# Optimization experiments

Hardware: AMD Instinct MI355X
Metric: run time of the kernel (lower is better)

Reference implementation:

```python
import jax, jax.numpy as jnp
import numpy as np

N_EXPERTS = 8
TOP_K = 2
D_MODEL = 1024
N_TOKENS = 8192


def setup_inputs() -> dict:
    key = jax.random.key(0)
    k1, k2, k3, k4, k5 = jax.random.split(key, 5)
    x = jax.random.normal(k1, (N_TOKENS, D_MODEL), dtype=jnp.float32)
    # router Linear(num_experts): weight [d, E], bias [E]
    Wr = jax.random.normal(k2, (D_MODEL, N_EXPERTS), dtype=jnp.float32) / np.sqrt(D_MODEL)
    br = jnp.zeros((N_EXPERTS,), dtype=jnp.float32)
    # per-expert Linear(d_model): stacked weights [E, d, d], biases [E, d]
    W = jax.random.normal(k3, (N_EXPERTS, D_MODEL, D_MODEL), dtype=jnp.float32) / np.sqrt(D_MODEL)
    b = jnp.zeros((N_EXPERTS, D_MODEL), dtype=jnp.float32)
    return {"x": x, "Wr": Wr, "br": br, "W": W, "b": b}


def reference(x, Wr, br, W, b):
    # --- route ---
    logits = x @ Wr + br                                  # [N, E]
    top_k_vals, top_k_idxs = jax.lax.top_k(logits, TOP_K)  # [N, k]
    top_k_gates = jax.nn.softmax(top_k_vals, axis=-1)      # [N, k]
    # --- experts (dense form of gather-dispatch; same math as routed compute) ---
    y_all = jnp.einsum('nd,edh->neh', x, W) + b            # [N, E, d]
    # --- gather routed expert outputs per slot ---
    y_k = jnp.take_along_axis(y_all, top_k_idxs[:, :, None], axis=1)  # [N, k, d]
    # --- weighted scatter-combine (reduce) ---
    out = jnp.sum(top_k_gates[:, :, None] * y_k, axis=1)   # [N, d]
    return out
```

## Files before the change

kernel.cpp:

```cpp
#include <hip/hip_runtime.h>
#include <hip/hip_bf16.h>


#define NTOK 8192
#define DM   1024
#define NEXP 8
#define CAP  8192
#define MAXT 136

typedef __attribute__((ext_vector_type(8))) short bf16x8;
typedef __attribute__((ext_vector_type(4))) float f32x4;

__device__ __forceinline__ unsigned short f2bf(float f) {
  unsigned u = __float_as_uint(f);
  unsigned r = (u + 0x7fffu + ((u >> 16) & 1u)) >> 16;
  return (unsigned short)r;
}
__device__ __forceinline__ float bf2f(unsigned short s) {
  return __uint_as_float(((unsigned)s) << 16);
}

__device__ __forceinline__ void gl_lds16(const void* g, void* l) {
  __builtin_amdgcn_global_load_lds(
      (const __attribute__((address_space(1))) unsigned int*)g,
      (__attribute__((address_space(3))) unsigned int*)l, 16, 0, 0);
}

__global__ __launch_bounds__(256) void transpose_w_kernel(
    const float* __restrict__ W, unsigned short* __restrict__ Wt) {
  __shared__ unsigned short L[64 * 260];
  const int e = blockIdx.z;
  const int d0 = blockIdx.y * 256, h0 = blockIdx.x * 64;
  const float* Ws = W + (size_t)e * DM * DM;
  unsigned short* Wd = Wt + (size_t)e * DM * DM;
  const int tid = threadIdx.x;
  const int hh = (tid & 15) * 4;
  const int dr = tid >> 4;
#pragma unroll
  for (int it = 0; it < 16; it++) {
    int dd = it * 16 + dr;
    float4 v = *(const float4*)(Ws + (size_t)(d0 + dd) * DM + h0 + hh);
    L[(hh + 0) * 260 + dd] = f2bf(v.x);
    L[(hh + 1) * 260 + dd] = f2bf(v.y);
    L[(hh + 2) * 260 + dd] = f2bf(v.z);
    L[(hh + 3) * 260 + dd] = f2bf(v.w);
  }
  __syncthreads();
  const int dc = (tid & 63) * 4;
  const int hw = tid >> 6;
#pragma unroll
  for (int it = 0; it < 16; it++) {
    int hr = it * 4 + hw;
    ushort4 o = *(const ushort4*)(&L[hr * 260 + dc]);
    *(ushort4*)(Wd + (size_t)(h0 + hr) * DM + d0 + dc) = o;
  }
}

__global__ __launch_bounds__(256) void router_compute_kernel(
    const float* __restrict__ x, const float* __restrict__ Wr,
    const float* __restrict__ br, unsigned short* __restrict__ xbf,
    int4* __restrict__ topk) {
  const int tid = threadIdx.x;
  const int wave = tid >> 6, lane = tid & 63;
  const int t = blockIdx.x * 4 + wave;
  const int c0 = lane * 16;
  const float* xr = x + (size_t)t * DM + c0;

  float v[16];
#pragma unroll
  for (int i = 0; i < 4; i++) {
    float4 f = *(const float4*)(xr + i * 4);
    v[i * 4 + 0] = f.x; v[i * 4 + 1] = f.y; v[i * 4 + 2] = f.z; v[i * 4 + 3] = f.w;
  }
  union { unsigned short s[8]; uint4 q; } pk;
#pragma unroll
  for (int half = 0; half < 2; half++) {
#pragma unroll
    for (int i = 0; i < 8; i++) pk.s[i] = f2bf(v[half * 8 + i]);
    *(uint4*)(xbf + (size_t)t * DM + c0 + half * 8) = pk.q;
  }
  float p[8] = {0, 0, 0, 0, 0, 0, 0, 0};
  const float* wr = Wr + (size_t)c0 * NEXP;
#pragma unroll
  for (int i = 0; i < 16; i++) {
    float xv = v[i];
    float4 wl = *(const float4*)(wr + i * 8);
    float4 wh = *(const float4*)(wr + i * 8 + 4);
    p[0] += xv * wl.x; p[1] += xv * wl.y; p[2] += xv * wl.z; p[3] += xv * wl.w;
    p[4] += xv * wh.x; p[5] += xv * wh.y; p[6] += xv * wh.z; p[7] += xv * wh.w;
  }
#pragma unroll
  for (int off = 32; off >= 1; off >>= 1) {
#pragma unroll
    for (int e = 0; e < 8; e++) p[e] += __shfl_xor(p[e], off, 64);
  }
  if (lane == 0) {
    float lg[8];
#pragma unroll
    for (int e = 0; e < 8; e++) lg[e] = p[e] + br[e];
    float v0 = lg[0]; int i0 = 0;
#pragma unroll
    for (int e = 1; e < 8; e++) if (lg[e] > v0) { v0 = lg[e]; i0 = e; }
    float v1 = -3.4e38f; int i1 = 0;
#pragma unroll
    for (int e = 0; e < 8; e++)
      if (e != i0 && lg[e] > v1) { v1 = lg[e]; i1 = e; }
    float ee = __expf(v1 - v0);
    float g0 = 1.0f / (1.0f + ee);
    float g1 = ee / (1.0f + ee);
    int4 rec;
    rec.x = i0; rec.y = i1;
    rec.z = __float_as_int(g0); rec.w = __float_as_int(g1);
    topk[t] = rec;
  }
}

__global__ __launch_bounds__(512) void scatter_kernel(
    const int4* __restrict__ topk, int* __restrict__ counts,
    int* __restrict__ tok, int2* __restrict__ pos) {
  __shared__ int lcnt[NEXP], lbase[NEXP];
  const int tid = threadIdx.x;
  if (tid < NEXP) lcnt[tid] = 0;
  __syncthreads();
  const int t = blockIdx.x * 512 + tid;
  int4 r = topk[t];
  int s0 = atomicAdd(&lcnt[r.x], 1);
  int s1 = atomicAdd(&lcnt[r.y], 1);
  __syncthreads();
  if (tid < NEXP) lbase[tid] = atomicAdd(&counts[tid], lcnt[tid]);
  __syncthreads();
  int p0 = lbase[r.x] + s0;
  int p1 = lbase[r.y] + s1;
  tok[r.x * CAP + p0] = t;
  tok[r.y * CAP + p1] = t;
  int2 pr; pr.x = p0; pr.y = p1;
  pos[t] = pr;
}

__global__ __launch_bounds__(64) void build_tiles_kernel(
    const int* __restrict__ counts, int* __restrict__ desc,
    int* __restrict__ ntiles, int* __restrict__ offset) {
  if (threadIdx.x == 0) {
    int idx = 0, off = 0;
#pragma unroll
    for (int e = 0; e < NEXP; e++) {
      offset[e] = off;
      off += counts[e];
      int nm = (counts[e] + 127) >> 7;
      for (int i = 0; i < nm; i++) desc[idx++] = (e << 16) | i;
    }
    *ntiles = idx;
  }
}

__global__ __launch_bounds__(256) void moe_gemm_kernel(
    const unsigned short* __restrict__ xbf, const unsigned short* __restrict__ wt,
    const int* __restrict__ counts, const int* __restrict__ offset,
    const int* __restrict__ tok, const int* __restrict__ desc,
    const int* __restrict__ ntiles, unsigned short* __restrict__ ybuf) {
  const int slot = blockIdx.x;
  if (slot >= *ntiles) return;
  const int dsc = desc[slot];
  const int e = dsc >> 16;
  const int m0 = (dsc & 0xffff) * 128;
  const int cnt = counts[e];
  const int n0 = blockIdx.y * 128;

  __shared__ __align__(16) unsigned short sA0[128 * 32];
  __shared__ __align__(16) unsigned short sB0[128 * 32];
  __shared__ __align__(16) unsigned short sA1[128 * 32];
  __shared__ __align__(16) unsigned short sB1[128 * 32];

  const int tid = threadIdx.x, wave = tid >> 6, lane = tid & 63;

  const int rA1 = wave * 16 + (lane >> 2);
  const int rA2 = rA1 + 64;
  const int cch = lane & 3;
  const int cg1 = (cch ^ ((rA1 >> 1) & 3)) * 8;
  const int cg2 = (cch ^ ((rA2 >> 1) & 3)) * 8;
  int r1 = m0 + rA1; if (r1 >= cnt) r1 = cnt - 1;
  int r2 = m0 + rA2; if (r2 >= cnt) r2 = cnt - 1;
  const int t1 = tok[e * CAP + r1];
  const int t2 = tok[e * CAP + r2];
  const unsigned short* pA1 = xbf + (size_t)t1 * DM + cg1;
  const unsigned short* pA2 = xbf + (size_t)t2 * DM + cg2;
  const unsigned short* wte = wt + (size_t)e * DM * DM;
  const unsigned short* pB1 = wte + (size_t)(n0 + rA1) * DM + cg1;
  const unsigned short* pB2 = wte + (size_t)(n0 + rA2) * DM + cg2;
  const int lo1 = wave * 512, lo2 = (wave + 4) * 512;

  const int q = lane >> 4, ml = lane & 15;
  const int wm = (wave >> 1) * 64, wn = (wave & 1) * 64;
  int offA[4], offB[4];
#pragma unroll
  for (int i = 0; i < 4; i++) {
    int row = wm + i * 16 + ml;
    offA[i] = row * 32 + (q ^ ((row >> 1) & 3)) * 8;
    int rowb = wn + i * 16 + ml;
    offB[i] = rowb * 32 + (q ^ ((rowb >> 1) & 3)) * 8;
  }

  f32x4 acc[4][4] = {};

  for (int k0 = 0; k0 < DM; k0 += 64) {
    gl_lds16(pA1 + k0, sA0 + lo1);
    gl_lds16(pA2 + k0, sA0 + lo2);
    gl_lds16(pB1 + k0, sB0 + lo1);
    gl_lds16(pB2 + k0, sB0 + lo2);
    gl_lds16(pA1 + k0 + 32, sA1 + lo1);
    gl_lds16(pA2 + k0 + 32, sA1 + lo2);
    gl_lds16(pB1 + k0 + 32, sB1 + lo1);
    gl_lds16(pB2 + k0 + 32, sB1 + lo2);
    __syncthreads();
    bf16x8 af0[4], bf0[4], af1[4], bf1[4];
#pragma unroll
    for (int i = 0; i < 4; i++) {
      af0[i] = *(const bf16x8*)(sA0 + offA[i]);
      bf0[i] = *(const bf16x8*)(sB0 + offB[i]);
      af1[i] = *(const bf16x8*)(sA1 + offA[i]);
      bf1[i] = *(const bf16x8*)(sB1 + offB[i]);
    }
#pragma unroll
    for (int mt = 0; mt < 4; mt++)
#pragma unroll
      for (int nt = 0; nt < 4; nt++)
        acc[mt][nt] = __builtin_amdgcn_mfma_f32_16x16x32_bf16(
            af0[mt], bf0[nt], acc[mt][nt], 0, 0, 0);
#pragma unroll
    for (int mt = 0; mt < 4; mt++)
#pragma unroll
      for (int nt = 0; nt < 4; nt++)
        acc[mt][nt] = __builtin_amdgcn_mfma_f32_16x16x32_bf16(
            af1[mt], bf1[nt], acc[mt][nt], 0, 0, 0);
    __syncthreads();
  }

  const int yb = offset[e] + m0;
#pragma unroll
  for (int mt = 0; mt < 4; mt++) {
    int rbase = wm + mt * 16 + q * 4;
#pragma unroll
    for (int r = 0; r < 4; r++) {
      int row = rbase + r;
      if (m0 + row >= cnt) continue;
      unsigned short* yrow = ybuf + (size_t)(yb + row) * DM + n0;
#pragma unroll
      for (int nt = 0; nt < 4; nt++) {
        yrow[wn + nt * 16 + ml] = f2bf(acc[mt][nt][r]);
      }
    }
  }
}

__global__ __launch_bounds__(256) void combine_kernel(
    const unsigned short* __restrict__ ybuf, const int4* __restrict__ topk,
    const int2* __restrict__ pos, const int* __restrict__ offset,
    const float* __restrict__ bias, float* __restrict__ out) {
  const int t = blockIdx.x;
  const int c = threadIdx.x * 4;
  int4 r = topk[t];
  int2 p = pos[t];
  float g0 = __int_as_float(r.z), g1 = __int_as_float(r.w);
  int s0 = offset[r.x] + p.x;
  int s1 = offset[r.y] + p.y;
  ushort4 ya = *(const ushort4*)(ybuf + (size_t)s0 * DM + c);
  ushort4 yb = *(const ushort4*)(ybuf + (size_t)s1 * DM + c);
  float4 b0 = *(const float4*)(bias + (size_t)r.x * DM + c);
  float4 b1 = *(const float4*)(bias + (size_t)r.y * DM + c);
  float4 o;
  o.x = g0 * (bf2f(ya.x) + b0.x) + g1 * (bf2f(yb.x) + b1.x);
  o.y = g0 * (bf2f(ya.y) + b0.y) + g1 * (bf2f(yb.y) + b1.y);
  o.z = g0 * (bf2f(ya.z) + b0.z) + g1 * (bf2f(yb.z) + b1.z);
  o.w = g0 * (bf2f(ya.w) + b0.w) + g1 * (bf2f(yb.w) + b1.w);
  *(float4*)(out + (size_t)t * DM + c) = o;
}

extern "C" void kernel_launch(void* const* d_in, const int* in_sizes, int n_in,
                              void* d_out, int out_size, void* d_ws, size_t ws_size,
                              hipStream_t stream) {
  const float* x  = (const float*)d_in[0];
  const float* Wr = (const float*)d_in[1];
  const float* br = (const float*)d_in[2];
  const float* W  = (const float*)d_in[3];
  const float* b  = (const float*)d_in[4];
  float* out = (float*)d_out;

  char* ws = (char*)d_ws;
  unsigned short* xbf  = (unsigned short*)ws;
  unsigned short* wt   = (unsigned short*)(ws + (16u << 20));
  unsigned short* ybuf = (unsigned short*)(ws + (32u << 20));
  char* ctrl = ws + (64u << 20);
  int*   counts = (int*)ctrl;
  int*   ntiles = (int*)(ctrl + 64);
  int*   offset = (int*)(ctrl + 128);
  int*   desc   = (int*)(ctrl + 256);
  int*   tok    = (int*)(ctrl + 4096);
  int2*  pos    = (int2*)(ctrl + 4096 + (256u << 10));
  int4*  topk   = (int4*)(ctrl + 4096 + (320u << 10));

  hipMemsetAsync(counts, 0, 128, stream);

  transpose_w_kernel<<<dim3(16, 4, 8), 256, 0, stream>>>(W, wt);
  router_compute_kernel<<<NTOK / 4, 256, 0, stream>>>(x, Wr, br, xbf, topk);
  scatter_kernel<<<16, 512, 0, stream>>>(topk, counts, tok, pos);
  build_tiles_kernel<<<1, 64, 0, stream>>>(counts, desc, ntiles, offset);
  moe_gemm_kernel<<<dim3(MAXT, 8), 256, 0, stream>>>(
      xbf, wt, counts, offset, tok, desc, ntiles, ybuf);
  combine_kernel<<<NTOK, 256, 0, stream>>>(ybuf, topk, pos, offset, b, out);
}
```

Measured before the change: 215.1 us.

## Fuse prepass kernels, drop memset and tile-build launch, compute offsets inline

Merges the weight transpose/convert and router into a single prepass kernel, which also clears the expert counts, replacing a memset and two launches. The tile descriptor build kernel is removed: each GEMM block derives its expert, row offset and output base directly from counts. The combine kernel computes offsets from counts itself and assigns one wave per token. The GEMM grid is reordered so consecutive blocks share an M-tile. This cuts launch count and serial tiny kernels, at the cost of redundant per-block prefix computations.

After: 215.1 us. About the same (-0.0%).

```diff
diff --git a/kernel.cpp b/kernel.cpp
--- a/kernel.cpp
+++ b/kernel.cpp
@@ -26,43 +26,48 @@
       (__attribute__((address_space(3))) unsigned int*)l, 16, 0, 0);
 }
 
-__global__ __launch_bounds__(256) void transpose_w_kernel(
-    const float* __restrict__ W, unsigned short* __restrict__ Wt) {
-  __shared__ unsigned short L[64 * 260];
-  const int e = blockIdx.z;
-  const int d0 = blockIdx.y * 256, h0 = blockIdx.x * 64;
-  const float* Ws = W + (size_t)e * DM * DM;
-  unsigned short* Wd = Wt + (size_t)e * DM * DM;
-  const int tid = threadIdx.x;
-  const int hh = (tid & 15) * 4;
-  const int dr = tid >> 4;
-#pragma unroll
-  for (int it = 0; it < 16; it++) {
-    int dd = it * 16 + dr;
-    float4 v = *(const float4*)(Ws + (size_t)(d0 + dd) * DM + h0 + hh);
-    L[(hh + 0) * 260 + dd] = f2bf(v.x);
-    L[(hh + 1) * 260 + dd] = f2bf(v.y);
-    L[(hh + 2) * 260 + dd] = f2bf(v.z);
-    L[(hh + 3) * 260 + dd] = f2bf(v.w);
-  }
-  __syncthreads();
-  const int dc = (tid & 63) * 4;
-  const int hw = tid >> 6;
-#pragma unroll
-  for (int it = 0; it < 16; it++) {
-    int hr = it * 4 + hw;
-    ushort4 o = *(const ushort4*)(&L[hr * 260 + dc]);
-    *(ushort4*)(Wd + (size_t)(h0 + hr) * DM + d0 + dc) = o;
-  }
-}
-
-__global__ __launch_bounds__(256) void router_compute_kernel(
+__global__ __launch_bounds__(256) void prepass_kernel(
+    const float* __restrict__ W, unsigned short* __restrict__ Wt,
     const float* __restrict__ x, const float* __restrict__ Wr,
     const float* __restrict__ br, unsigned short* __restrict__ xbf,
-    int4* __restrict__ topk) {
+    int4* __restrict__ topk, int* __restrict__ counts) {
+  __shared__ unsigned short L[64 * 132];
+  const int bx = blockIdx.x;
   const int tid = threadIdx.x;
+
+  if (bx == 0 && tid < NEXP) counts[tid] = 0;
+
+  if (bx < 1024) {
+    const int e = bx & 7;
+    const int d0 = ((bx >> 3) & 7) * 128;
+    const int h0 = (bx >> 6) * 64;
+    const float* Ws = W + (size_t)e * DM * DM;
+    unsigned short* Wd = Wt + (size_t)e * DM * DM;
+    const int hh = (tid & 15) * 4;
+    const int dr = tid >> 4;
+#pragma unroll
+    for (int it = 0; it < 8; it++) {
+      int dd = it * 16 + dr;
+      float4 v = *(const float4*)(Ws + (size_t)(d0 + dd) * DM + h0 + hh);
+      L[(hh + 0) * 132 + dd] = f2bf(v.x);
+      L[(hh + 1) * 132 + dd] = f2bf(v.y);
+      L[(hh + 2) * 132 + dd] = f2bf(v.z);
+      L[(hh + 3) * 132 + dd] = f2bf(v.w);
+    }
+    __syncthreads();
+    const int dc = (tid & 31) * 4;
+    const int hw = tid >> 5;
+#pragma unroll
+    for (int it = 0; it < 8; it++) {
+      int hr = it * 8 + hw;
+      ushort4 o = *(const ushort4*)(&L[hr * 132 + dc]);
+      *(ushort4*)(Wd + (size_t)(h0 + hr) * DM + d0 + dc) = o;
+    }
+    return;
+  }
+
   const int wave = tid >> 6, lane = tid & 63;
-  const int t = blockIdx.x * 4 + wave;
+  const int t = (bx - 1024) * 4 + wave;
   const int c0 = lane * 16;
   const float* xr = x + (size_t)t * DM + c0;
 
@@ -137,34 +142,26 @@
   pos[t] = pr;
 }
 
-__global__ __launch_bounds__(64) void build_tiles_kernel(
-    const int* __restrict__ counts, int* __restrict__ desc,
-    int* __restrict__ ntiles, int* __restrict__ offset) {
-  if (threadIdx.x == 0) {
-    int idx = 0, off = 0;
-#pragma unroll
-    for (int e = 0; e < NEXP; e++) {
-      offset[e] = off;
-      off += counts[e];
-      int nm = (counts[e] + 127) >> 7;
-      for (int i = 0; i < nm; i++) desc[idx++] = (e << 16) | i;
-    }
-    *ntiles = idx;
-  }
-}
-
 __global__ __launch_bounds__(256) void moe_gemm_kernel(
     const unsigned short* __restrict__ xbf, const unsigned short* __restrict__ wt,
-    const int* __restrict__ counts, const int* __restrict__ offset,
-    const int* __restrict__ tok, const int* __restrict__ desc,
-    const int* __restrict__ ntiles, unsigned short* __restrict__ ybuf) {
-  const int slot = blockIdx.x;
-  if (slot >= *ntiles) return;
-  const int dsc = desc[slot];
-  const int e = dsc >> 16;
-  const int m0 = (dsc & 0xffff) * 128;
-  const int cnt = counts[e];
-  const int n0 = blockIdx.y * 128;
+    const int* __restrict__ counts, const int* __restrict__ tok,
+    unsigned short* __restrict__ ybuf) {
+  const int slot = blockIdx.y;
+  int e = 0, m0 = 0, yb0 = 0, cnt = 0;
+  {
+    int tacc = 0, oacc = 0, found = 0;
+#pragma unroll
+    for (int ee = 0; ee < NEXP; ee++) {
+      int c = counts[ee];
+      int nm = (c + 127) >> 7;
+      if (!found && slot < tacc + nm) {
+        e = ee; m0 = (slot - tacc) * 128; yb0 = oacc; cnt = c; found = 1;
+      }
+      tacc += nm; oacc += c;
+    }
+    if (!found) return;
+  }
+  const int n0 = blockIdx.x * 128;
 
   __shared__ __align__(16) unsigned short sA0[128 * 32];
   __shared__ __align__(16) unsigned short sB0[128 * 32];
@@ -235,7 +232,7 @@
     __syncthreads();
   }
 
-  const int yb = offset[e] + m0;
+  const int yb = yb0 + m0;
 #pragma unroll
   for (int mt = 0; mt < 4; mt++) {
     int rbase = wm + mt * 16 + q * 4;
@@ -254,25 +251,40 @@
 
 __global__ __launch_bounds__(256) void combine_kernel(
     const unsigned short* __restrict__ ybuf, const int4* __restrict__ topk,
-    const int2* __restrict__ pos, const int* __restrict__ offset,
+    const int2* __restrict__ pos, const int* __restrict__ counts,
     const float* __restrict__ bias, float* __restrict__ out) {
-  const int t = blockIdx.x;
-  const int c = threadIdx.x * 4;
+  const int tid = threadIdx.x;
+  const int wave = tid >> 6, lane = tid & 63;
+  const int t = blockIdx.x * 4 + wave;
   int4 r = topk[t];
   int2 p = pos[t];
+  int off0 = 0, off1 = 0;
+#pragma unroll
+  for (int e = 0; e < NEXP; e++) {
+    int c = counts[e];
+    if (e < r.x) off0 += c;
+    if (e < r.y) off1 += c;
+  }
   float g0 = __int_as_float(r.z), g1 = __int_as_float(r.w);
-  int s0 = offset[r.x] + p.x;
-  int s1 = offset[r.y] + p.y;
-  ushort4 ya = *(const ushort4*)(ybuf + (size_t)s0 * DM + c);
-  ushort4 yb = *(const ushort4*)(ybuf + (size_t)s1 * DM + c);
-  float4 b0 = *(const float4*)(bias + (size_t)r.x * DM + c);
-  float4 b1 = *(const float4*)(bias + (size_t)r.y * DM + c);
-  float4 o;
-  o.x = g0 * (bf2f(ya.x) + b0.x) + g1 * (bf2f(yb.x) + b1.x);
-  o.y = g0 * (bf2f(ya.y) + b0.y) + g1 * (bf2f(yb.y) + b1.y);
-  o.z = g0 * (bf2f(ya.z) + b0.z) + g1 * (bf2f(yb.z) + b1.z);
-  o.w = g0 * (bf2f(ya.w) + b0.w) + g1 * (bf2f(yb.w) + b1.w);
-  *(float4*)(out + (size_t)t * DM + c) = o;
+  const unsigned short* y0 = ybuf + (size_t)(off0 + p.x) * DM + lane * 16;
+  const unsigned short* y1 = ybuf + (size_t)(off1 + p.y) * DM + lane * 16;
+  const float* b0 = bias + (size_t)r.x * DM + lane * 16;
+  const float* b1 = bias + (size_t)r.y * DM + lane * 16;
+  float* orow = out + (size_t)t * DM + lane * 16;
+  union { ushort4 u4; unsigned short s[4]; } ya, yb;
+#pragma unroll
+  for (int j = 0; j < 4; j++) {
+    ya.u4 = *(const ushort4*)(y0 + j * 4);
+    yb.u4 = *(const ushort4*)(y1 + j * 4);
+    float4 c0 = *(const float4*)(b0 + j * 4);
+    float4 c1 = *(const float4*)(b1 + j * 4);
+    float4 o;
+    o.x = g0 * (bf2f(ya.s[0]) + c0.x) + g1 * (bf2f(yb.s[0]) + c1.x);
+    o.y = g0 * (bf2f(ya.s[1]) + c0.y) + g1 * (bf2f(yb.s[1]) + c1.y);
+    o.z = g0 * (bf2f(ya.s[2]) + c0.z) + g1 * (bf2f(yb.s[2]) + c1.z);
+    o.w = g0 * (bf2f(ya.s[3]) + c0.w) + g1 * (bf2f(yb.s[3]) + c1.w);
+    *(float4*)(orow + j * 4) = o;
+  }
 }
 
 extern "C" void kernel_launch(void* const* d_in, const int* in_sizes, int n_in,
@@ -291,20 +303,15 @@
   unsigned short* ybuf = (unsigned short*)(ws + (32u << 20));
   char* ctrl = ws + (64u << 20);
   int*   counts = (int*)ctrl;
-  int*   ntiles = (int*)(ctrl + 64);
-  int*   offset = (int*)(ctrl + 128);
-  int*   desc   = (int*)(ctrl + 256);
   int*   tok    = (int*)(ctrl + 4096);
   int2*  pos    = (int2*)(ctrl + 4096 + (256u << 10));
   int4*  topk   = (int4*)(ctrl + 4096 + (320u << 10));
 
-  hipMemsetAsync(counts, 0, 128, stream);
-
-  transpose_w_kernel<<<dim3(16, 4, 8), 256, 0, stream>>>(W, wt);
-  router_compute_kernel<<<NTOK / 4, 256, 0, stream>>>(x, Wr, br, xbf, topk);
+  prepass_kernel<<<1024 + NTOK / 4, 256, 0, stream>>>(
+      W, wt, x, Wr, br, xbf, topk, counts);
   scatter_kernel<<<16, 512, 0, stream>>>(topk, counts, tok, pos);
-  build_tiles_kernel<<<1, 64, 0, stream>>>(counts, desc, ntiles, offset);
-  moe_gemm_kernel<<<dim3(MAXT, 8), 256, 0, stream>>>(
-      xbf, wt, counts, offset, tok, desc, ntiles, ybuf);
-  combine_kernel<<<NTOK, 256, 0, stream>>>(ybuf, topk, pos, offset, b, out);
-}
+  moe_gemm_kernel<<<dim3(8, MAXT), 256, 0, stream>>>(
+      xbf, wt, counts, tok, ybuf);
+  combine_kernel<<<NTOK / 4, 256, 0, stream>>>(
+      ybuf, topk, pos, counts, b, out);
+}
```
